# Kernel tuning notes

Measured on AMD Instinct MI355X. Metric: run time of the kernel, lower is better.

The kernel has to match this reference:

```python
import jax, jax.numpy as jnp
import numpy as np

B, S, E = 2, 2048, 2048
H = 16
KV_RANK = 512
ROPE = 64
NOPE = 64  # source sets qk_nope_dim = qk_rope_dim
VD = 128   # v_head_dim = head_dim
QD = ROPE + NOPE  # q_head_dim = 128


def setup_inputs() -> dict:
    key = jax.random.key(0)
    ks = jax.random.split(key, 5)
    sd = lambda fan_in: 1.0 / np.sqrt(fan_in)
    return {
        "x": jax.random.normal(ks[0], (B, S, E), jnp.float32),
        "attention_mask": jnp.zeros((1, 1, S, S), jnp.float32),
        "W_kv_down": jax.random.normal(ks[1], (KV_RANK + ROPE, E), jnp.float32) * sd(E),
        "W_kv_up": jax.random.normal(ks[2], (H * (VD + NOPE), KV_RANK), jnp.float32) * sd(KV_RANK),
        "W_q": jax.random.normal(ks[3], (H * QD, E), jnp.float32) * sd(E),
        "W_out": jax.random.normal(ks[4], (E, H * VD), jnp.float32) * sd(H * VD),
    }


def reference(x, attention_mask, W_kv_down, W_kv_up, W_q, W_out):
    scale = QD ** (-0.5)
    # down-project to latent + rope part
    compressed = jnp.einsum('bse,fe->bsf', x, W_kv_down)          # [B,S,KV_RANK+ROPE]
    kv_c, k_rope = compressed[..., :KV_RANK], compressed[..., KV_RANK:]
    # up-project latent to per-head v and k_nope
    kv_exp = jnp.einsum('bsr,fr->bsf', kv_c, W_kv_up)             # [B,S,H*(VD+NOPE)]
    kv_exp = kv_exp.reshape(B, S, H, VD + NOPE).transpose(0, 2, 1, 3)  # [B,H,S,VD+NOPE]
    v, k_nope = kv_exp[..., :VD], kv_exp[..., VD:]
    # shared rope key broadcast over heads, concat [rope, nope]
    k_rope_b = jnp.broadcast_to(k_rope[:, None], (B, H, S, ROPE))
    k = jnp.concatenate([k_rope_b, k_nope], axis=-1)              # [B,H,S,QD]
    # queries
    q = jnp.einsum('bse,fe->bsf', x, W_q).reshape(B, S, H, QD).transpose(0, 2, 1, 3)
    scores = jnp.einsum('bhsd,bhtd->bhst', q, k) * scale + attention_mask
    w = jax.nn.softmax(scores, axis=-1)
    out = jnp.einsum('bhst,bhtv->bhsv', w, v)                     # [B,H,S,VD]
    out = out.transpose(0, 2, 1, 3).reshape(B, S, H * VD)
    return jnp.einsum('bsf,ef->bse', out, W_out)
```

## Files before the change

### kernel.cpp

```cpp
#include <hip/hip_runtime.h>
#include <hip/hip_bf16.h>
#include <stdint.h>

typedef __bf16 bf16x8 __attribute__((ext_vector_type(8)));
typedef float f32x4 __attribute__((ext_vector_type(4)));
typedef float f32x16 __attribute__((ext_vector_type(16)));
typedef uint32_t u32x4 __attribute__((ext_vector_type(4)));
typedef unsigned short ushort_t;
typedef unsigned short ushort8v __attribute__((ext_vector_type(8)));

#define MFMA16 __builtin_amdgcn_mfma_f32_16x16x32_bf16
#define MFMA32 __builtin_amdgcn_mfma_f32_32x32x16_bf16

static constexpr int Bc = 2, Sc = 2048, Ec = 2048, Hc = 16;

__device__ __forceinline__ void gload16(const void* g, void* l) {
  __builtin_amdgcn_global_load_lds(
      (const __attribute__((address_space(1))) void*)g,
      (__attribute__((address_space(3))) void*)l, 16, 0, 0);
}

__device__ __forceinline__ ushort_t f2bf(float f) {
  uint32_t u = __float_as_uint(f);
  uint32_t r = (u + 0x7fffu + ((u >> 16) & 1u)) >> 16;
  return (ushort_t)r;
}
__device__ __forceinline__ float bf2f(ushort_t u) {
  return __uint_as_float((uint32_t)u << 16);
}
__device__ __forceinline__ uint32_t cvtpk(float a, float b) {
  uint32_t d;
  asm("v_cvt_pk_bf16_f32 %0, %1, %2" : "=v"(d) : "v"(a), "v"(b));
  return d;
}
__device__ __forceinline__ void plswap(uint32_t& a, uint32_t& b) {
  asm("v_permlane32_swap_b32 %0, %1" : "+v"(a), "+v"(b));
}

__global__ void cast_all(const float* __restrict__ x, const float* __restrict__ Wq,
                         const float* __restrict__ Wkvu, const float* __restrict__ Wout,
                         const float* __restrict__ Wkvd,
                         ushort_t* __restrict__ xb, ushort_t* __restrict__ wq,
                         ushort_t* __restrict__ wkvu, ushort_t* __restrict__ wout,
                         ushort_t* __restrict__ wkvd) {
  int i = blockIdx.x * 256 + threadIdx.x;
  const float* src;
  ushort_t* dst;
  int j;
  if (i < 2097152) { src = x; dst = xb; j = i; }
  else if (i < 3145728) { src = Wq; dst = wq; j = i - 2097152; }
  else if (i < 3538944) { src = Wkvu; dst = wkvu; j = i - 3145728; }
  else if (i < 4587520) { src = Wout; dst = wout; j = i - 3538944; }
  else {
    j = i - 4587520;
    int row = j >> 9, col4 = j & 511;
    ushort4 o;
    if (row < 576) {
      float4 v = ((const float4*)Wkvd)[row * 512 + col4];
      o.x = f2bf(v.x); o.y = f2bf(v.y); o.z = f2bf(v.z); o.w = f2bf(v.w);
    } else { o.x = 0; o.y = 0; o.z = 0; o.w = 0; }
    ((ushort4*)wkvd)[j] = o;
    return;
  }
  float4 v = ((const float4*)src)[j];
  ushort4 o;
  o.x = f2bf(v.x); o.y = f2bf(v.y); o.z = f2bf(v.z); o.w = f2bf(v.w);
  ((ushort4*)dst)[j] = o;
}

__global__ void prep_kernel(const float* __restrict__ mask, ushort_t* __restrict__ m4,
                            const ushort_t* __restrict__ comp, char* __restrict__ kbuf) {
  const float INVLN2 = 1.4426950408889634f;
  int gb = blockIdx.x;
  if (gb < 2048) {
    int i = gb * 256 + threadIdx.x;
    int rr = i & 1, half = (i >> 1) & 1, kblk = (i >> 2) & 1, kt = (i >> 3) & 31, q = i >> 8;
    const float* src = mask + (size_t)q * 2048 + kt * 64 + kblk * 32 + half * 4 + rr * 16;
    float4 a = *(const float4*)src;
    float4 c = *(const float4*)(src + 8);
    ushort8v o;
    o[0] = f2bf(a.x * INVLN2); o[1] = f2bf(a.y * INVLN2);
    o[2] = f2bf(a.z * INVLN2); o[3] = f2bf(a.w * INVLN2);
    o[4] = f2bf(c.x * INVLN2); o[5] = f2bf(c.y * INVLN2);
    o[6] = f2bf(c.z * INVLN2); o[7] = f2bf(c.w * INVLN2);
    size_t u5 = ((((size_t)(q >> 5) * 32 + kt) * 4 + kblk * 2 + rr) * 64) + half * 32 + (q & 31);
    ((ushort8v*)m4)[u5] = o;
  } else {
    int i = (gb - 2048) * 256 + threadIdx.x;
    int blk = i & 7;
    int m = i >> 3;
    int s = m & 2047, b = m >> 11;
    uint4 v = *(const uint4*)&comp[(size_t)m * 640 + 512 + blk * 8];
    int kt = s >> 6, kblk = (s & 63) >> 5;
    size_t base = (size_t)kt * 16384 + kblk * 8192 + (blk >> 1) * 1024 +
                  ((blk & 1) * 32 + (s & 31)) * 16;
#pragma unroll
    for (int h = 0; h < Hc; h++) {
      *(uint4*)(kbuf + (size_t)(b * Hc + h) * 524288 + base) = v;
    }
  }
}

template<int MODE>
__global__ __launch_bounds__(256, 2)
void gemm_bt(const ushort_t* __restrict__ A, int lda,
             const ushort_t* __restrict__ Bm, int ldb,
             void* __restrict__ Cout, int ldc,
             int M, int N, int K,
             char* __restrict__ vtb, char* __restrict__ kbuf)
{
  __shared__ __align__(16) ushort_t sA[2][128 * 32];
  __shared__ __align__(16) ushort_t sB[2][128 * 32];
  int tid = threadIdx.x;
  int nTn = N >> 7;
  int bid = blockIdx.x;
  int chunk = gridDim.x >> 3;
  bid = (bid & 7) * chunk + (bid >> 3);
  int tm = bid / nTn, tn = bid - tm * nTn;
  int wave = tid >> 6, lane = tid & 63;
  int wm = (wave >> 1) << 6, wn = (wave & 1) << 6;
  int l16 = lane & 15, g16 = lane >> 4;
  f32x4 acc[4][4] = {};
  int srow = tid >> 2, scol = (tid & 3) << 3;
  const ushort_t* Ag = A + (size_t)(tm * 128 + srow) * lda + scol;
  const ushort_t* Bg = Bm + (size_t)(tn * 128 + srow) * ldb + scol;
  ushort_t* sA0 = &sA[0][srow * 32 + scol];
  ushort_t* sA1 = &sA[1][srow * 32 + scol];
  ushort_t* sB0 = &sB[0][srow * 32 + scol];
  ushort_t* sB1 = &sB[1][srow * 32 + scol];
  for (int kt = 0; kt < K; kt += 64) {
    gload16(Ag, sA0);
    gload16(Ag + (size_t)64 * lda, sA0 + 64 * 32);
    gload16(Ag + 32, sA1);
    gload16(Ag + (size_t)64 * lda + 32, sA1 + 64 * 32);
    gload16(Bg, sB0);
    gload16(Bg + (size_t)64 * ldb, sB0 + 64 * 32);
    gload16(Bg + 32, sB1);
    gload16(Bg + (size_t)64 * ldb + 32, sB1 + 64 * 32);
    Ag += 64; Bg += 64;
    __syncthreads();
#pragma unroll
    for (int h2 = 0; h2 < 2; h2++) {
      bf16x8 af[4], bfr[4];
#pragma unroll
      for (int i = 0; i < 4; i++) af[i] = *(const bf16x8*)&sA[h2][(wm + i * 16 + l16) * 32 + g16 * 8];
#pragma unroll
      for (int i = 0; i < 4; i++) bfr[i] = *(const bf16x8*)&sB[h2][(wn + i * 16 + l16) * 32 + g16 * 8];
#pragma unroll
      for (int i = 0; i < 4; i++)
#pragma unroll
        for (int j = 0; j < 4; j++)
          acc[i][j] = MFMA16(af[i], bfr[j], acc[i][j], 0, 0, 0);
    }
    __syncthreads();
  }
#pragma unroll
  for (int i = 0; i < 4; i++) {
#pragma unroll
    for (int j = 0; j < 4; j++) {
      int grow0 = tm * 128 + wm + i * 16 + g16 * 4;
      int gcol = tn * 128 + wn + j * 16 + l16;
      if constexpr (MODE == 0) {
#pragma unroll
        for (int r = 0; r < 4; r++)
          ((ushort_t*)Cout)[(size_t)(grow0 + r) * ldc + gcol] = f2bf(acc[i][j][r]);
      } else if constexpr (MODE == 2) {
#pragma unroll
        for (int r = 0; r < 4; r++)
          ((float*)Cout)[(size_t)(grow0 + r) * ldc + gcol] = acc[i][j][r];
      } else {
        int h = gcol / 192, jj = gcol - h * 192;
        int b = grow0 >> 11, s0 = grow0 & 2047;
        size_t bh = (size_t)(b * Hc + h);
        int kt = s0 >> 6, sl = s0 & 63;
        int kblk = sl >> 5, l32s = sl & 31;
        if (jj < 128) {
          int k2 = (sl >> 4) & 1, halfv = (sl >> 3) & 1, e0 = sl & 7;
          ushort4 pk;
          pk.x = f2bf(acc[i][j][0]); pk.y = f2bf(acc[i][j][1]);
          pk.z = f2bf(acc[i][j][2]); pk.w = f2bf(acc[i][j][3]);
          *(ushort4*)(vtb + bh * 524288 + (size_t)kt * 16384 + kblk * 8192 + k2 * 4096 +
                      (jj >> 5) * 1024 + (halfv * 32 + (jj & 31)) * 16 + e0 * 2) = pk;
        } else {
          int qd = jj - 64;
          int ks = qd >> 4, halfq = (qd >> 3) & 1, e = qd & 7;
          char* kp = kbuf + bh * 524288 + (size_t)kt * 16384 + kblk * 8192 + ks * 1024 +
                     (halfq * 32 + l32s) * 16 + e * 2;
#pragma unroll
          for (int r = 0; r < 4; r++)
            *(ushort_t*)(kp + r * 16) = f2bf(acc[i][j][r]);
        }
      }
    }
  }
}

__global__ __launch_bounds__(64, 2)
void attn_kernel(const ushort_t* __restrict__ qb, const char* __restrict__ kbuf,
                 const char* __restrict__ vtb, const ushort_t* __restrict__ m4,
                 ushort_t* __restrict__ attn_o)
{
  const float scale2 = 0.12752081738040466f;
  int bid = blockIdx.x;
  bid = (bid & 7) * 256 + (bid >> 3);
  int qt = bid & 63, bh = bid >> 6;
  int b = bh >> 4, h = bh & 15;
  int l = threadIdx.x, l32 = l & 31, half = l >> 5;
  int qbase = qt * 32;

  bf16x8 qf[8];
  {
    const ushort_t* qp = qb + (size_t)(b * Sc + qbase + l32) * 2048 + h * 128 + half * 8;
#pragma unroll
    for (int ks = 0; ks < 8; ks++) qf[ks] = *(const bf16x8*)(qp + ks * 16);
  }

  float mrun = -3.0e38f, lrun = 0.f;
  f32x16 acco[4] = {};

  const char* kg = kbuf + (size_t)bh * 524288;
  const char* vg = vtb + (size_t)bh * 524288;
  const ushort8v* mbase = (const ushort8v*)m4 + (size_t)qt * 8192;
  int moff = half * 32 + l32;

  bf16x8 kfA[8], kfB[8];
  {
    const char* p = kg + l * 16;
#pragma unroll
    for (int ks = 0; ks < 8; ks++) kfA[ks] = *(const bf16x8*)(p + ks * 1024);
  }

  auto PHASE = [&](int kt, int kblk, bf16x8 (&kfc)[8], bf16x8 (&kfn)[8],
                   int ktn, int nkblk) {
    bf16x8 vv[8];
    {
      const char* p = vg + (size_t)kt * 16384 + kblk * 8192 + l * 16;
#pragma unroll
      for (int i2 = 0; i2 < 8; i2++) vv[i2] = *(const bf16x8*)(p + i2 * 1024);
    }
    ushort8v mca = mbase[(kt * 4 + kblk * 2) * 64 + moff];
    ushort8v mcb = mbase[(kt * 4 + kblk * 2 + 1) * 64 + moff];

    f32x16 sc = {};
    __builtin_amdgcn_s_setprio(1);
#pragma unroll
    for (int ks = 0; ks < 8; ks++) sc = MFMA32(kfc[ks], qf[ks], sc, 0, 0, 0);
    __builtin_amdgcn_s_setprio(0);

    {
      const char* p = kg + (size_t)ktn * 16384 + nkblk * 8192 + l * 16;
#pragma unroll
      for (int ks = 0; ks < 8; ks++) kfn[ks] = *(const bf16x8*)(p + ks * 1024);
    }

#pragma unroll
    for (int r = 0; r < 16; r++)
      sc[r] = sc[r] * scale2 + bf2f((r < 8 ? mca : mcb)[r & 7]);
    float mx = sc[0];
#pragma unroll
    for (int r = 1; r < 16; r++) mx = fmaxf(mx, sc[r]);
    mx = fmaxf(mx, __shfl_xor(mx, 32));
    if (!__all(mx <= mrun + 11.0f)) {
      float mnew = fmaxf(mrun, mx);
      float corr = __builtin_amdgcn_exp2f(mrun - mnew);
      lrun *= corr; mrun = mnew;
#pragma unroll
      for (int r = 0; r < 16; r++) {
        float cr = __shfl(corr, (r & 3) + 8 * (r >> 2) + 4 * half);
#pragma unroll
        for (int vb = 0; vb < 4; vb++) acco[vb][r] *= cr;
      }
    }
    float rs = 0.f;
    uint32_t W[8];
#pragma unroll
    for (int m = 0; m < 4; m++) {
      float p0 = __builtin_amdgcn_exp2f(sc[4 * m + 0] - mrun);
      float p1 = __builtin_amdgcn_exp2f(sc[4 * m + 1] - mrun);
      float p2 = __builtin_amdgcn_exp2f(sc[4 * m + 2] - mrun);
      float p3 = __builtin_amdgcn_exp2f(sc[4 * m + 3] - mrun);
      rs += (p0 + p1) + (p2 + p3);
      W[2 * m] = cvtpk(p0, p1);
      W[2 * m + 1] = cvtpk(p2, p3);
    }
    lrun += rs;

    bf16x8 pf[2];
#pragma unroll
    for (int k2 = 0; k2 < 2; k2++) {
      uint32_t a0 = W[4 * k2 + 0], a1 = W[4 * k2 + 1];
      uint32_t b0 = W[4 * k2 + 2], b1 = W[4 * k2 + 3];
      plswap(a0, b0);
      plswap(a1, b1);
      u32x4 t; t[0] = a0; t[1] = a1; t[2] = b0; t[3] = b1;
      pf[k2] = __builtin_bit_cast(bf16x8, t);
    }

    __builtin_amdgcn_s_setprio(1);
#pragma unroll
    for (int k2 = 0; k2 < 2; k2++)
#pragma unroll
      for (int vb = 0; vb < 4; vb++)
        acco[vb] = MFMA32(pf[k2], vv[k2 * 4 + vb], acco[vb], 0, 0, 0);
    __builtin_amdgcn_s_setprio(0);
  };

#pragma unroll 1
  for (int kt = 0; kt < 32; kt++) {
    PHASE(kt, 0, kfA, kfB, kt, 1);
    PHASE(kt, 1, kfB, kfA, (kt + 1) & 31, 0);
  }

  lrun += __shfl_xor(lrun, 32);
#pragma unroll
  for (int r = 0; r < 16; r++) {
    int rowq = (r & 3) + 8 * (r >> 2) + 4 * half;
    float lr = __shfl(lrun, rowq);
    float inv = 1.0f / lr;
    int qrow = qbase + rowq;
    ushort_t* op = attn_o + (size_t)(b * Sc + qrow) * 2048 + h * 128 + l32;
#pragma unroll
    for (int vb = 0; vb < 4; vb++)
      op[vb * 32] = f2bf(acco[vb][r] * inv);
  }
}

extern "C" void kernel_launch(void* const* d_in, const int* in_sizes, int n_in,
                              void* d_out, int out_size, void* d_ws, size_t ws_size,
                              hipStream_t stream) {
  const float* x    = (const float*)d_in[0];
  const float* mask = (const float*)d_in[1];
  const float* Wkvd = (const float*)d_in[2];
  const float* Wkvu = (const float*)d_in[3];
  const float* Wq   = (const float*)d_in[4];
  const float* Wout = (const float*)d_in[5];

  char* ws = (char*)d_ws;
  size_t off = 0;
  auto alloc = [&](size_t bytes) { char* p = ws + off; off += (bytes + 255) & ~(size_t)255; return p; };
  ushort_t* xb   = (ushort_t*)alloc((size_t)4096 * 2048 * 2);
  ushort_t* wkvd = (ushort_t*)alloc((size_t)640 * 2048 * 2);
  ushort_t* wq   = (ushort_t*)alloc((size_t)2048 * 2048 * 2);
  ushort_t* wkvu = (ushort_t*)alloc((size_t)3072 * 512 * 2);
  ushort_t* wout = (ushort_t*)alloc((size_t)2048 * 2048 * 2);
  ushort_t* comp = (ushort_t*)alloc((size_t)4096 * 640 * 2);
  ushort_t* qbuf = (ushort_t*)alloc((size_t)4096 * 2048 * 2);
  char*     kbuf = alloc((size_t)Bc * Hc * Sc * 256);
  char*     vtb  = alloc((size_t)Bc * Hc * 524288);
  ushort_t* attn_o = xb;
  ushort_t* m4 = wq;

  cast_all<<<19200, 256, 0, stream>>>(x, Wq, Wkvu, Wout, Wkvd, xb, wq, wkvu, wout, wkvd);

  gemm_bt<0><<<32 * 5, 256, 0, stream>>>(xb, 2048, wkvd, 2048, comp, 640, 4096, 640, 2048, nullptr, nullptr);
  gemm_bt<0><<<32 * 16, 256, 0, stream>>>(xb, 2048, wq, 2048, qbuf, 2048, 4096, 2048, 2048, nullptr, nullptr);
  prep_kernel<<<2176, 256, 0, stream>>>(mask, m4, comp, kbuf);
  gemm_bt<1><<<32 * 24, 256, 0, stream>>>(comp, 640, wkvu, 512, nullptr, 0, 4096, 3072, 512, vtb, kbuf);
  attn_kernel<<<2048, 64, 0, stream>>>(qbuf, kbuf, vtb, m4, attn_o);
  gemm_bt<2><<<32 * 16, 256, 0, stream>>>(attn_o, 2048, wout, 2048, d_out, 2048, 4096, 2048, 2048, nullptr, nullptr);
}
```

Measured before the change: 267.3 us.

## Split attention key range across two waves per block with LDS merge

```diff
diff --git a/kernel.cpp b/kernel.cpp
--- a/kernel.cpp
+++ b/kernel.cpp
@@ -195,17 +195,21 @@
   }
 }
 
-__global__ __launch_bounds__(64, 2)
+__global__ __launch_bounds__(128, 3)
 void attn_kernel(const ushort_t* __restrict__ qb, const char* __restrict__ kbuf,
                  const char* __restrict__ vtb, const ushort_t* __restrict__ m4,
                  ushort_t* __restrict__ attn_o)
 {
+  __shared__ float sO[32 * 128];
+  __shared__ float sM[64];
+  __shared__ float sL[32];
   const float scale2 = 0.12752081738040466f;
   int bid = blockIdx.x;
   bid = (bid & 7) * 256 + (bid >> 3);
   int qt = bid & 63, bh = bid >> 6;
   int b = bh >> 4, h = bh & 15;
-  int l = threadIdx.x, l32 = l & 31, half = l >> 5;
+  int tid = threadIdx.x, wave = tid >> 6, l = tid & 63;
+  int l32 = l & 31, half = l >> 5;
   int qbase = qt * 32;
 
   bf16x8 qf[8];
@@ -225,7 +229,7 @@
 
   bf16x8 kfA[8], kfB[8];
   {
-    const char* p = kg + l * 16;
+    const char* p = kg + (size_t)(wave * 16) * 16384 + l * 16;
 #pragma unroll
     for (int ks = 0; ks < 8; ks++) kfA[ks] = *(const bf16x8*)(p + ks * 1024);
   }
@@ -306,22 +310,47 @@
   };
 
 #pragma unroll 1
-  for (int kt = 0; kt < 32; kt++) {
+  for (int kt0 = 0; kt0 < 16; kt0++) {
+    int kt = wave * 16 + kt0;
     PHASE(kt, 0, kfA, kfB, kt, 1);
     PHASE(kt, 1, kfB, kfA, (kt + 1) & 31, 0);
   }
 
   lrun += __shfl_xor(lrun, 32);
-#pragma unroll
-  for (int r = 0; r < 16; r++) {
-    int rowq = (r & 3) + 8 * (r >> 2) + 4 * half;
-    float lr = __shfl(lrun, rowq);
-    float inv = 1.0f / lr;
-    int qrow = qbase + rowq;
-    ushort_t* op = attn_o + (size_t)(b * Sc + qrow) * 2048 + h * 128 + l32;
-#pragma unroll
-    for (int vb = 0; vb < 4; vb++)
-      op[vb * 32] = f2bf(acco[vb][r] * inv);
+  if (l < 32) sM[wave * 32 + l] = mrun;
+  __syncthreads();
+  float mOther = sM[(wave ^ 1) * 32 + l32];
+  float mStar = fmaxf(mrun, mOther);
+  float cw = __builtin_amdgcn_exp2f(mrun - mStar);
+  float lw = lrun * cw;
+
+  if (wave == 1) {
+#pragma unroll
+    for (int r = 0; r < 16; r++) {
+      int rowq = (r & 3) + 8 * (r >> 2) + 4 * half;
+      float cr = __shfl(cw, rowq);
+#pragma unroll
+      for (int vb = 0; vb < 4; vb++)
+        sO[rowq * 128 + vb * 32 + l32] = acco[vb][r] * cr;
+    }
+    if (l < 32) sL[l] = lw;
+  }
+  __syncthreads();
+  if (wave == 0) {
+#pragma unroll
+    for (int r = 0; r < 16; r++) {
+      int rowq = (r & 3) + 8 * (r >> 2) + 4 * half;
+      float cr = __shfl(cw, rowq);
+      float ltot = __shfl(lw, rowq) + sL[rowq];
+      float inv = 1.0f / ltot;
+      int qrow = qbase + rowq;
+      ushort_t* op = attn_o + (size_t)(b * Sc + qrow) * 2048 + h * 128 + l32;
+#pragma unroll
+      for (int vb = 0; vb < 4; vb++) {
+        float o = acco[vb][r] * cr + sO[rowq * 128 + vb * 32 + l32];
+        op[vb * 32] = f2bf(o * inv);
+      }
+    }
   }
 }
 
@@ -356,6 +385,6 @@
   gemm_bt<0><<<32 * 16, 256, 0, stream>>>(xb, 2048, wq, 2048, qbuf, 2048, 4096, 2048, 2048, nullptr, nullptr);
   prep_kernel<<<2176, 256, 0, stream>>>(mask, m4, comp, kbuf);
   gemm_bt<1><<<32 * 24, 256, 0, stream>>>(comp, 640, wkvu, 512, nullptr, 0, 4096, 3072, 512, vtb, kbuf);
-  attn_kernel<<<2048, 64, 0, stream>>>(qbuf, kbuf, vtb, m4, attn_o);
+  attn_kernel<<<2048, 128, 0, stream>>>(qbuf, kbuf, vtb, m4, attn_o);
   gemm_bt<2><<<32 * 16, 256, 0, stream>>>(attn_o, 2048, wout, 2048, d_out, 2048, 4096, 2048, 2048, nullptr, nullptr);
 }
```

Measured after the change: 491.9 us. +84.0%, slower.
